# Kernel optimization log

Hardware: AMD Instinct MI355X
Metric: run time of the kernel (lower is better)

The kernel has to match this reference:

```python
import jax, jax.numpy as jnp
import numpy as np

B, S, H, E, V = 256, 512, 512, 128, 30000
RNN_IN = H + E + 1  # weighted context + id embedding + rate


def setup_inputs() -> dict:
    key = jax.random.key(0)
    ks = jax.random.split(key, 16)
    nrm = lambda k, shape, s=0.02: jax.random.normal(k, shape, dtype=jnp.float32) * s
    return {
        "input_id": jax.random.randint(ks[0], (B, 1), 0, V),
        "input_rate": jax.random.uniform(ks[1], (B, 1), dtype=jnp.float32),
        "hidden": nrm(ks[2], (1, B, H), 1.0),
        "encoder_outputs": nrm(ks[3], (S, B, H), 1.0),
        "attn_mask": jax.random.randint(ks[4], (B, S), 0, 2),
        "constraint_vec": (jax.random.uniform(ks[5], (B, V)) > 0.3).astype(jnp.float32),
        "emb_id": nrm(ks[6], (V, E)),
        "attn_w": nrm(ks[7], (2 * H, H)),
        "attn_b": jnp.zeros((H,), jnp.float32),
        "v_w": nrm(ks[8], (H,)),
        "w_ih": nrm(ks[9], (3 * H, RNN_IN)),
        "w_hh": nrm(ks[10], (3 * H, H)),
        "b_ih": jnp.zeros((3 * H,), jnp.float32),
        "b_hh": jnp.zeros((3 * H,), jnp.float32),
        "fc_id_w": nrm(ks[11], (H, V)),
        "fc_id_b": jnp.zeros((V,), jnp.float32),
        "tandem_w": nrm(ks[12], (E + H, H)),
        "tandem_b": jnp.zeros((H,), jnp.float32),
        "rate_w": nrm(ks[13], (H, 1)),
        "rate_b": jnp.zeros((1,), jnp.float32),
    }


def reference(input_id, input_rate, hidden, encoder_outputs, attn_mask,
              constraint_vec, emb_id, attn_w, attn_b, v_w,
              w_ih, w_hh, b_ih, b_hh, fc_id_w, fc_id_b,
              tandem_w, tandem_b, rate_w, rate_b):
    hd = hidden.shape[-1]
    h0 = hidden[0]                                # [B, H]
    embedded = emb_id[input_id[:, 0]]             # [B, E] (dropout p=0 -> identity)

    # --- additive attention (concat-linear split to avoid [B,S,2H] concat) ---
    enc = jnp.transpose(encoder_outputs, (1, 0, 2))         # [B, S, H]
    hid_part = h0 @ attn_w[:hd]                             # [B, H]
    enc_part = jnp.einsum('bsh,hk->bsk', enc, attn_w[hd:])  # [B, S, H]
    energy = jnp.tanh(hid_part[:, None, :] + enc_part + attn_b)
    scores = jnp.einsum('bsh,h->bs', energy, v_w)           # [B, S]
    scores = jnp.where(attn_mask == 0, jnp.float32(-1e10), scores)
    a = jax.nn.softmax(scores, axis=1)
    weighted = jnp.einsum('bs,bsh->bh', a, enc)             # [B, H]

    # --- GRU cell (torch gate order: r, z, n) ---
    x = jnp.concatenate([weighted, embedded, input_rate], axis=1)  # [B, H+E+1]
    gi = x @ w_ih.T + b_ih
    gh = h0 @ w_hh.T + b_hh
    gi_r, gi_z, gi_n = jnp.split(gi, 3, axis=1)
    gh_r, gh_z, gh_n = jnp.split(gh, 3, axis=1)
    r = jax.nn.sigmoid(gi_r + gh_r)
    z = jax.nn.sigmoid(gi_z + gh_z)
    n = jnp.tanh(gi_n + r * gh_n)
    h1 = (1.0 - z) * n + z * h0                   # [B, H]

    # --- masked log-softmax over id vocabulary ---
    logits = h1 @ fc_id_w + fc_id_b               # [B, V]
    maxes = jnp.max(logits, axis=1, keepdims=True)
    x_exp = jnp.exp(logits - maxes) * constraint_vec
    pred = jnp.clip(x_exp / jnp.sum(x_exp, axis=1, keepdims=True), 1e-6, 1.0)
    prediction_id = jnp.log(pred)

    # --- tandem rate head ---
    max_id = jnp.argmax(prediction_id, axis=1)
    id_emb = emb_id[max_id]                       # [B, E]
    rate_in = jax.nn.relu(jnp.concatenate([id_emb, h1], axis=1) @ tandem_w + tandem_b)
    prediction_rate = jax.nn.sigmoid(rate_in @ rate_w + rate_b)  # [B, 1]

    return prediction_id, prediction_rate, h1[None]  # hidden [1, B, H]
```

## Files before the change

kernel.cpp:

```cpp
#include <hip/hip_runtime.h>
#include <hip/hip_bf16.h>

#define B_ 256
#define S_ 512
#define H_ 512
#define E_ 128
#define V_ 30000
#define RNNIN_ 641

using bf16x8 = __attribute__((ext_vector_type(8))) short;
using f32x4  = __attribute__((ext_vector_type(4))) float;

__device__ __forceinline__ short f2bf(float f) {
  unsigned int u = __float_as_uint(f);
  u += 0x7fffu + ((u >> 16) & 1u);
  return (short)(u >> 16);
}

__device__ __forceinline__ float fast_tanh(float x) {
  x = fminf(10.f, fmaxf(-10.f, x));
  float t = __expf(2.f * x);
  return (t - 1.f) / (t + 1.f);
}

__device__ __forceinline__ float sigmoidf(float x) {
  return 1.f / (1.f + __expf(-x));
}

__device__ __forceinline__ void gload_lds16(const void* g, void* l) {
  __builtin_amdgcn_global_load_lds(
      (const __attribute__((address_space(1))) void*)g,
      (__attribute__((address_space(3))) void*)l, 16, 0, 0);
}

__global__ __launch_bounds__(256) void pack_b(
    const float* __restrict__ in, unsigned short* __restrict__ out)
{
  int i = blockIdx.x * 256 + threadIdx.x;
  int k = i >> 9, n = i & 511;
  float v = in[i];
  int idx = ((((k >> 5) * 32 + (n >> 4)) * 4 + ((k >> 3) & 3)) * 16 + (n & 15)) * 8 + (k & 7);
  out[idx] = (unsigned short)f2bf(v);
}

template<bool BT, bool RELU>
__global__ __launch_bounds__(256) void gemm_f32(
    const float* __restrict__ A, const float* __restrict__ Bm,
    const float* __restrict__ bias, float* __restrict__ C,
    int M, int N, int K)
{
  __shared__ float As[16][65];
  __shared__ float Bs[16][65];
  const int m0 = blockIdx.x * 64, n0 = blockIdx.y * 64;
  const int tid = threadIdx.x;
  const int tx = tid & 15, ty = tid >> 4;
  float acc[4][4] = {};
  for (int k0 = 0; k0 < K; k0 += 16) {
    __syncthreads();
    #pragma unroll
    for (int i = 0; i < 4; i++) {
      int e = tid + i * 256;
      int m = e >> 4, k = e & 15;
      float v = 0.f;
      if (m0 + m < M && k0 + k < K) v = A[(size_t)(m0 + m) * K + k0 + k];
      As[k][m] = v;
    }
    #pragma unroll
    for (int i = 0; i < 4; i++) {
      int e = tid + i * 256;
      if (BT) {
        int n = e >> 4, k = e & 15;
        float v = 0.f;
        if (n0 + n < N && k0 + k < K) v = Bm[(size_t)(n0 + n) * K + k0 + k];
        Bs[k][n] = v;
      } else {
        int k = e >> 6, n = e & 63;
        float v = 0.f;
        if (n0 + n < N && k0 + k < K) v = Bm[(size_t)(k0 + k) * N + n0 + n];
        Bs[k][n] = v;
      }
    }
    __syncthreads();
    #pragma unroll
    for (int k = 0; k < 16; k++) {
      float a[4], b[4];
      #pragma unroll
      for (int i = 0; i < 4; i++) a[i] = As[k][ty * 4 + i];
      #pragma unroll
      for (int j = 0; j < 4; j++) b[j] = Bs[k][tx * 4 + j];
      #pragma unroll
      for (int i = 0; i < 4; i++)
        #pragma unroll
        for (int j = 0; j < 4; j++) acc[i][j] += a[i] * b[j];
    }
  }
  #pragma unroll
  for (int i = 0; i < 4; i++) {
    int m = m0 + ty * 4 + i;
    if (m >= M) continue;
    #pragma unroll
    for (int j = 0; j < 4; j++) {
      int n = n0 + tx * 4 + j;
      if (n >= N) continue;
      float v = acc[i][j] + (bias ? bias[n] : 0.f);
      if (RELU) v = fmaxf(v, 0.f);
      C[(size_t)m * N + n] = v;
    }
  }
}

__device__ void gemm_bt_dev(float (*As)[65], float (*Bs)[65],
    const float* __restrict__ A, const float* __restrict__ Bm,
    const float* __restrict__ bias, float* __restrict__ C,
    int M, int N, int K)
{
  const int m0 = blockIdx.x * 64, n0 = blockIdx.y * 64;
  const int tid = threadIdx.x;
  const int tx = tid & 15, ty = tid >> 4;
  float acc[4][4] = {};
  for (int k0 = 0; k0 < K; k0 += 16) {
    __syncthreads();
    #pragma unroll
    for (int i = 0; i < 4; i++) {
      int e = tid + i * 256;
      int m = e >> 4, k = e & 15;
      float v = 0.f;
      if (m0 + m < M && k0 + k < K) v = A[(size_t)(m0 + m) * K + k0 + k];
      As[k][m] = v;
    }
    #pragma unroll
    for (int i = 0; i < 4; i++) {
      int e = tid + i * 256;
      int n = e >> 4, k = e & 15;
      float v = 0.f;
      if (n0 + n < N && k0 + k < K) v = Bm[(size_t)(n0 + n) * K + k0 + k];
      Bs[k][n] = v;
    }
    __syncthreads();
    #pragma unroll
    for (int k = 0; k < 16; k++) {
      float a[4], b[4];
      #pragma unroll
      for (int i = 0; i < 4; i++) a[i] = As[k][ty * 4 + i];
      #pragma unroll
      for (int j = 0; j < 4; j++) b[j] = Bs[k][tx * 4 + j];
      #pragma unroll
      for (int i = 0; i < 4; i++)
        #pragma unroll
        for (int j = 0; j < 4; j++) acc[i][j] += a[i] * b[j];
    }
  }
  #pragma unroll
  for (int i = 0; i < 4; i++) {
    int m = m0 + ty * 4 + i;
    if (m >= M) continue;
    #pragma unroll
    for (int j = 0; j < 4; j++) {
      int n = n0 + tx * 4 + j;
      if (n >= N) continue;
      C[(size_t)m * N + n] = acc[i][j] + bias[n];
    }
  }
}

__global__ __launch_bounds__(256) void gemm_gru(
    const float* __restrict__ xb, const float* __restrict__ w_ih,
    const float* __restrict__ b_ih, float* __restrict__ gi,
    const float* __restrict__ hid, const float* __restrict__ w_hh,
    const float* __restrict__ b_hh, float* __restrict__ gh)
{
  __shared__ float As[16][65];
  __shared__ float Bs[16][65];
  if (blockIdx.z == 0) gemm_bt_dev(As, Bs, xb, w_ih, b_ih, gi, B_, 1536, RNNIN_);
  else                 gemm_bt_dev(As, Bs, hid, w_hh, b_hh, gh, B_, 1536, H_);
}

__global__ __launch_bounds__(256, 3) void attn_gemm_score(
    const float* __restrict__ A, const unsigned short* __restrict__ Btf,
    const float* __restrict__ hid_pb, const float* __restrict__ v_w,
    float* __restrict__ scores)
{
  __shared__ short As[2 * 4 * 64 * 8];
  __shared__ short Bs[2 * 16 * 64 * 8];

  const int bid  = blockIdx.x;
  const int tile = (bid & 7) * 512 + (bid >> 3);
  const int mblk = tile >> 1, nblk = tile & 1;
  const int m0 = mblk * 64, n0 = nblk * 256;

  const int tid  = threadIdx.x;
  const int lane = tid & 63;
  const int wv   = tid >> 6;
  const int quad = lane >> 4, l15 = lane & 15;

  const int arow = tid >> 2;
  const int aseg = tid & 3;
  const float* aptr = A + (size_t)(m0 + arow) * H_ + aseg * 16;
  const int ac = aseg >> 1, aq0 = (aseg & 1) * 2;
  short* aw0 = &As[((ac * 4 + (arow >> 4)) * 64 + aq0 * 16 + (arow & 15)) * 8];
  short* aw1 = aw0 + 16 * 8;

  const unsigned short* bsrc = Btf + nblk * 8192;

  f32x4 acc[4][4];
  #pragma unroll
  for (int i = 0; i < 4; i++)
    #pragma unroll
    for (int j = 0; j < 4; j++) acc[i][j] = f32x4{0.f, 0.f, 0.f, 0.f};

  float4 rA[4];
  #pragma unroll
  for (int i = 0; i < 4; i++) rA[i] = *(const float4*)(aptr + i * 4);

  for (int kt = 0; kt < 8; kt++) {
    __builtin_amdgcn_s_barrier();
    asm volatile("s_waitcnt vmcnt(0)" ::: "memory");

    #pragma unroll
    for (int i = 0; i < 8; i++) {
      const unsigned short* g = bsrc + (kt * 2 + (i >> 2)) * 16384
                                     + ((i & 3) * 256 + tid) * 8;
      gload_lds16((const void*)g, (void*)&Bs[(i * 256 + wv * 64) * 8]);
    }

    {
      bf16x8 f0, f1;
      f0[0] = f2bf(rA[0].x); f0[1] = f2bf(rA[0].y); f0[2] = f2bf(rA[0].z); f0[3] = f2bf(rA[0].w);
      f0[4] = f2bf(rA[1].x); f0[5] = f2bf(rA[1].y); f0[6] = f2bf(rA[1].z); f0[7] = f2bf(rA[1].w);
      f1[0] = f2bf(rA[2].x); f1[1] = f2bf(rA[2].y); f1[2] = f2bf(rA[2].z); f1[3] = f2bf(rA[2].w);
      f1[4] = f2bf(rA[3].x); f1[5] = f2bf(rA[3].y); f1[6] = f2bf(rA[3].z); f1[7] = f2bf(rA[3].w);
      *(bf16x8*)aw0 = f0;
      *(bf16x8*)aw1 = f1;
    }

    if (kt < 7) {
      asm volatile("" ::: "memory");
      const float* anext = aptr + (kt + 1) * 64;
      #pragma unroll
      for (int i = 0; i < 4; i++) rA[i] = *(const float4*)(anext + i * 4);
      asm volatile("s_waitcnt vmcnt(4) lgkmcnt(0)" ::: "memory");
    } else {
      asm volatile("s_waitcnt vmcnt(0) lgkmcnt(0)" ::: "memory");
    }
    __builtin_amdgcn_s_barrier();
    asm volatile("" ::: "memory");

    #pragma unroll
    for (int ch = 0; ch < 2; ch++) {
      bf16x8 a[4], b[4];
      #pragma unroll
      for (int ti = 0; ti < 4; ti++)
        a[ti] = *(const bf16x8*)&As[((ch * 4 + ti) * 64 + lane) * 8];
      #pragma unroll
      for (int tj = 0; tj < 4; tj++)
        b[tj] = *(const bf16x8*)&Bs[((ch * 16 + wv * 4 + tj) * 64 + lane) * 8];
      #pragma unroll
      for (int ti = 0; ti < 4; ti++)
        #pragma unroll
        for (int tj = 0; tj < 4; tj++)
          acc[ti][tj] = __builtin_amdgcn_mfma_f32_16x16x32_bf16(a[ti], b[tj], acc[ti][tj], 0, 0, 0);
    }
  }

  __syncthreads();
  float* part = (float*)As;
  #pragma unroll
  for (int ti = 0; ti < 4; ti++) {
    #pragma unroll
    for (int r = 0; r < 4; r++) {
      int m = m0 + ti * 16 + quad * 4 + r;
      int b = m & (B_ - 1);
      float sum = 0.f;
      #pragma unroll
      for (int tj = 0; tj < 4; tj++) {
        int n = n0 + wv * 64 + tj * 16 + l15;
        float v = acc[ti][tj][r] + hid_pb[b * H_ + n];
        sum += fast_tanh(v) * v_w[n];
      }
      sum += __shfl_xor(sum, 1);
      sum += __shfl_xor(sum, 2);
      sum += __shfl_xor(sum, 4);
      sum += __shfl_xor(sum, 8);
      if (l15 == 0) part[(ti * 16 + quad * 4 + r) * 4 + wv] = sum;
    }
  }
  __syncthreads();
  if (tid < 64) {
    float s4 = part[tid * 4 + 0] + part[tid * 4 + 1] + part[tid * 4 + 2] + part[tid * 4 + 3];
    int m = m0 + tid;
    atomicAdd(scores + (m & (B_ - 1)) * S_ + (m >> 8), s4);
  }
}

__global__ __launch_bounds__(256, 4) void logits_gemm(
    const unsigned short* __restrict__ Ab, const float* __restrict__ Bw,
    const float* __restrict__ bias, float* __restrict__ C)
{
  __shared__ short As[2 * 16 * 64 * 8];
  __shared__ short Bs[2 * 4 * 64 * 8];
  const int n0 = blockIdx.x * 64;
  const int tid = threadIdx.x;
  const int lane = tid & 63;
  const int wv = tid >> 6;
  const int quad = lane >> 4, l15 = lane & 15;

  f32x4 acc[4][4];
  #pragma unroll
  for (int i = 0; i < 4; i++)
    #pragma unroll
    for (int j = 0; j < 4; j++) acc[i][j] = f32x4{0.f, 0.f, 0.f, 0.f};

  const int nB  = tid & 63;
  const int kg  = tid >> 6;
  const int cB  = kg >> 1;
  const int q0  = (kg & 1) * 2;
  const int tjB = nB >> 4;
  const bool nOK = (n0 + nB) < V_;

  for (int kt = 0; kt < 8; kt++) {
    const int kb = kt * 64;
    __syncthreads();
    #pragma unroll
    for (int p = 0; p < 8; p++) {
      int m = p * 32 + (tid >> 3), f = tid & 7;
      int c = f >> 2, q = f & 3;
      bf16x8 v = *(const bf16x8*)(Ab + (size_t)m * H_ + kb + c * 32 + q * 8);
      int mt = m >> 4, ld = q * 16 + (m & 15);
      *(bf16x8*)&As[((c * 16 + mt) * 64 + ld) * 8] = v;
    }
    {
      float col[16];
      const float* src = Bw + (size_t)(kb + kg * 16) * V_ + n0 + nB;
      #pragma unroll
      for (int i = 0; i < 16; i++) col[i] = nOK ? src[(size_t)i * V_] : 0.f;
      bf16x8 f0, f1;
      #pragma unroll
      for (int i = 0; i < 8; i++) { f0[i] = f2bf(col[i]); f1[i] = f2bf(col[8 + i]); }
      int ld0 = q0 * 16 + (nB & 15);
      *(bf16x8*)&Bs[((cB * 4 + tjB) * 64 + ld0) * 8] = f0;
      *(bf16x8*)&Bs[((cB * 4 + tjB) * 64 + ld0 + 16) * 8] = f1;
    }
    __syncthreads();
    #pragma unroll
    for (int c = 0; c < 2; c++) {
      bf16x8 a[4], b[4];
      #pragma unroll
      for (int ti = 0; ti < 4; ti++)
        a[ti] = *(const bf16x8*)&As[((c * 16 + wv * 4 + ti) * 64 + lane) * 8];
      #pragma unroll
      for (int tj = 0; tj < 4; tj++)
        b[tj] = *(const bf16x8*)&Bs[((c * 4 + tj) * 64 + lane) * 8];
      #pragma unroll
      for (int ti = 0; ti < 4; ti++)
        #pragma unroll
        for (int tj = 0; tj < 4; tj++)
          acc[ti][tj] = __builtin_amdgcn_mfma_f32_16x16x32_bf16(a[ti], b[tj], acc[ti][tj], 0, 0, 0);
    }
  }
  #pragma unroll
  for (int ti = 0; ti < 4; ti++)
    #pragma unroll
    for (int r = 0; r < 4; r++) {
      int m = wv * 64 + ti * 16 + quad * 4 + r;
      #pragma unroll
      for (int tj = 0; tj < 4; tj++) {
        int n = n0 + tj * 16 + l15;
        if (n < V_) C[(size_t)m * V_ + n] = acc[ti][tj][r] + bias[n];
      }
    }
}

__global__ __launch_bounds__(256) void attn_softmax(
    const float* __restrict__ scores, const int* __restrict__ mask, float* __restrict__ aw)
{
  int b = blockIdx.x, tid = threadIdx.x;
  __shared__ float red[256];
  float v0 = scores[b * S_ + tid];
  float v1 = scores[b * S_ + tid + 256];
  if (mask[b * S_ + tid] == 0) v0 = -1e10f;
  if (mask[b * S_ + tid + 256] == 0) v1 = -1e10f;
  red[tid] = fmaxf(v0, v1);
  __syncthreads();
  for (int off = 128; off; off >>= 1) { if (tid < off) red[tid] = fmaxf(red[tid], red[tid + off]); __syncthreads(); }
  float mx = red[0];
  __syncthreads();
  float e0 = __expf(v0 - mx), e1 = __expf(v1 - mx);
  red[tid] = e0 + e1;
  __syncthreads();
  for (int off = 128; off; off >>= 1) { if (tid < off) red[tid] += red[tid + off]; __syncthreads(); }
  float inv = 1.f / red[0];
  aw[b * S_ + tid] = e0 * inv;
  aw[b * S_ + tid + 256] = e1 * inv;
}

__global__ __launch_bounds__(512) void attn_weighted_part(
    const float* __restrict__ aw, const float* __restrict__ enc, float* __restrict__ wpart)
{
  int b = blockIdx.x, c = blockIdx.y, h = threadIdx.x;
  __shared__ float a_s[128];
  if (h < 128) a_s[h] = aw[b * S_ + c * 128 + h];
  __syncthreads();
  const float* ep = enc + ((size_t)(c * 128) * B_ + b) * H_ + h;
  float acc = 0.f;
  #pragma unroll 8
  for (int s = 0; s < 128; s++)
    acc += a_s[s] * ep[(size_t)s * B_ * H_];
  wpart[((size_t)c * B_ + b) * H_ + h] = acc;
}

__global__ void build_x(const float* __restrict__ wpart, const int* __restrict__ ids,
                        const float* __restrict__ emb, const float* __restrict__ rate,
                        float* __restrict__ x)
{
  int i = blockIdx.x * 256 + threadIdx.x;
  if (i >= B_ * RNNIN_) return;
  int b = i / RNNIN_, j = i % RNNIN_;
  float v;
  if (j < H_) {
    size_t o = (size_t)b * H_ + j;
    const size_t st = (size_t)B_ * H_;
    v = wpart[o] + wpart[o + st] + wpart[o + 2 * st] + wpart[o + 3 * st];
  }
  else if (j < H_ + E_) v = emb[(size_t)ids[b] * E_ + (j - H_)];
  else v = rate[b];
  x[i] = v;
}

__global__ void gru_gates(const float* __restrict__ gi, const float* __restrict__ gh,
                          const float* __restrict__ h0, float* __restrict__ h1,
                          unsigned short* __restrict__ h1b, float* __restrict__ h1_out)
{
  int i = blockIdx.x * 256 + threadIdx.x;
  int b = i >> 9, j = i & (H_ - 1);
  const float* gib = gi + (size_t)b * 1536;
  const float* ghb = gh + (size_t)b * 1536;
  float r = sigmoidf(gib[j] + ghb[j]);
  float z = sigmoidf(gib[512 + j] + ghb[512 + j]);
  float n = fast_tanh(gib[1024 + j] + r * ghb[1024 + j]);
  float h = (1.f - z) * n + z * h0[i];
  h1[i] = h;
  h1b[i] = (unsigned short)f2bf(h);
  h1_out[i] = h;
}

__global__ __launch_bounds__(1024) void softmax_fused(
    float* __restrict__ lp, const float* __restrict__ cv, int* __restrict__ maxid)
{
  int b = blockIdx.x, tid = threadIdx.x;
  int wid = tid >> 6, lane = tid & 63;
  float* row = lp + (size_t)b * V_;
  const float* cvr = cv + (size_t)b * V_;
  __shared__ float redf[16];
  __shared__ float rede[16];
  __shared__ int   redi[16];

  float mx = -INFINITY;
  for (int v = tid; v < V_; v += 1024) mx = fmaxf(mx, row[v]);
  #pragma unroll
  for (int o = 1; o < 64; o <<= 1) mx = fmaxf(mx, __shfl_xor(mx, o));
  if (lane == 0) redf[wid] = mx;
  __syncthreads();
  if (tid == 0) {
    float m = redf[0];
    for (int i = 1; i < 16; i++) m = fmaxf(m, redf[i]);
    redf[0] = m;
  }
  __syncthreads();
  float M = redf[0];
  __syncthreads();

  float s = 0.f, best = -1.f;
  int bi = 0;
  for (int v = tid; v < V_; v += 1024) {
    float e = __expf(row[v] - M) * cvr[v];
    row[v] = e;
    s += e;
    if (e > best) { best = e; bi = v; }
  }
  #pragma unroll
  for (int o = 1; o < 64; o <<= 1) {
    s += __shfl_xor(s, o);
    float ob = __shfl_xor(best, o);
    int oi = __shfl_xor(bi, o);
    if (ob > best || (ob == best && oi < bi)) { best = ob; bi = oi; }
  }
  if (lane == 0) { redf[wid] = s; rede[wid] = best; redi[wid] = bi; }
  __syncthreads();
  if (tid == 0) {
    float ss = 0.f, bb = rede[0];
    int ii = redi[0];
    for (int i = 0; i < 16; i++) {
      ss += redf[i];
      if (rede[i] > bb || (rede[i] == bb && redi[i] < ii)) { bb = rede[i]; ii = redi[i]; }
    }
    redf[0] = ss;
    maxid[b] = ii;
  }
  __syncthreads();
  float inv = 1.f / redf[0];
  for (int v = tid; v < V_; v += 1024) {
    float p = row[v] * inv;
    p = fminf(fmaxf(p, 1e-6f), 1.f);
    row[v] = __logf(p);
  }
}

__global__ void build_tandem(const int* __restrict__ maxid, const float* __restrict__ emb,
                             const float* __restrict__ h1, float* __restrict__ t)
{
  int i = blockIdx.x * 256 + threadIdx.x;
  if (i >= B_ * 640) return;
  int b = i / 640, j = i % 640;
  t[i] = (j < E_) ? emb[(size_t)maxid[b] * E_ + j] : h1[b * H_ + (j - E_)];
}

__global__ __launch_bounds__(64) void rate_head(const float* __restrict__ rate_in,
                                                const float* __restrict__ rate_w,
                                                const float* __restrict__ rate_b,
                                                float* __restrict__ out)
{
  int b = blockIdx.x, t = threadIdx.x;
  float s = 0.f;
  #pragma unroll
  for (int i = 0; i < 8; i++) s += rate_in[b * H_ + t + 64 * i] * rate_w[t + 64 * i];
  #pragma unroll
  for (int m = 32; m; m >>= 1) s += __shfl_xor(s, m);
  if (t == 0) out[b] = sigmoidf(s + rate_b[0]);
}

extern "C" void kernel_launch(void* const* d_in, const int* in_sizes, int n_in,
                              void* d_out, int out_size, void* d_ws, size_t ws_size,
                              hipStream_t stream)
{
  const int*   input_id   = (const int*)  d_in[0];
  const float* input_rate = (const float*)d_in[1];
  const float* hidden     = (const float*)d_in[2];
  const float* enc        = (const float*)d_in[3];
  const int*   attn_mask  = (const int*)  d_in[4];
  const float* cv         = (const float*)d_in[5];
  const float* emb        = (const float*)d_in[6];
  const float* attn_w     = (const float*)d_in[7];
  const float* attn_b     = (const float*)d_in[8];
  const float* v_w        = (const float*)d_in[9];
  const float* w_ih       = (const float*)d_in[10];
  const float* w_hh       = (const float*)d_in[11];
  const float* b_ih       = (const float*)d_in[12];
  const float* b_hh       = (const float*)d_in[13];
  const float* fc_w       = (const float*)d_in[14];
  const float* fc_b       = (const float*)d_in[15];
  const float* tan_w      = (const float*)d_in[16];
  const float* tan_b      = (const float*)d_in[17];
  const float* rate_w     = (const float*)d_in[18];
  const float* rate_b     = (const float*)d_in[19];

  float* out = (float*)d_out;
  float* ws  = (float*)d_ws;
  float* hid_pb   = ws;
  float* scores   = ws + 131072;
  float* aw       = ws + 262144;
  float* weighted = ws + 393216;
  float* xbuf     = ws + 524288;
  float* gi       = ws + 688384;
  float* gh       = ws + 1081600;
  float* h1       = ws + 1474816;
  float* rate_in  = ws + 1605888;
  int*   maxid    = (int*)(ws + 1736960);
  unsigned short* Btf = (unsigned short*)(ws + 1737216);
  unsigned short* h1b = (unsigned short*)(ws + 1868288);
  float* wpart = gi;

  float* out_pred = out;
  float* out_rate = out + (size_t)B_ * V_;
  float* out_h1   = out + (size_t)B_ * V_ + B_;
  (void)weighted;

  pack_b<<<1024, 256, 0, stream>>>(attn_w + (size_t)H_ * H_, Btf);

  hipMemsetAsync(scores, 0, (size_t)B_ * S_ * sizeof(float), stream);

  gemm_f32<false, false><<<dim3(4, 8), 256, 0, stream>>>(hidden, attn_w, attn_b, hid_pb, B_, H_, H_);

  attn_gemm_score<<<4096, 256, 0, stream>>>(enc, Btf, hid_pb, v_w, scores);

  attn_softmax<<<B_, 256, 0, stream>>>(scores, attn_mask, aw);
  attn_weighted_part<<<dim3(B_, 4), 512, 0, stream>>>(aw, enc, wpart);
  build_x<<<641, 256, 0, stream>>>(wpart, input_id, emb, input_rate, xbuf);

  gemm_gru<<<dim3(4, 24, 2), 256, 0, stream>>>(xbuf, w_ih, b_ih, gi, hidden, w_hh, b_hh, gh);
  gru_gates<<<512, 256, 0, stream>>>(gi, gh, hidden, h1, h1b, out_h1);

  logits_gemm<<<469, 256, 0, stream>>>(h1b, fc_w, fc_b, out_pred);
  softmax_fused<<<B_, 1024, 0, stream>>>(out_pred, cv, maxid);

  build_tandem<<<640, 256, 0, stream>>>(maxid, emb, h1, xbuf);
  gemm_f32<false, true><<<dim3(4, 8), 256, 0, stream>>>(xbuf, tan_w, tan_b, rate_in, B_, H_, 640);
  rate_head<<<B_, 64, 0, stream>>>(rate_in, rate_w, rate_b, out_rate);
}
```

Baseline: 1.042 ms.

## Fuse prep and tandem kernels, stream B from registers in attention GEMM

Merges the attn_w bf16 packing with the hidden-projection GEMM into one launch. It also folds the tandem input gather into the tandem GEMM, removing the xbuf round-trip and a launch. The attention-score GEMM now loads B fragments directly from global memory into registers instead of staging them in LDS. A is double-buffered in LDS so each k step needs only one barrier. The weighted-context reduction is split into 8 sequence chunks instead of 4 to raise parallelism, at the cost of summing more partial results.

Measured after the change: 1.004 ms. 3.6% less time.

```diff
diff --git a/kernel.cpp b/kernel.cpp
--- a/kernel.cpp
+++ b/kernel.cpp
@@ -27,31 +27,11 @@
   return 1.f / (1.f + __expf(-x));
 }
 
-__device__ __forceinline__ void gload_lds16(const void* g, void* l) {
-  __builtin_amdgcn_global_load_lds(
-      (const __attribute__((address_space(1))) void*)g,
-      (__attribute__((address_space(3))) void*)l, 16, 0, 0);
-}
-
-__global__ __launch_bounds__(256) void pack_b(
-    const float* __restrict__ in, unsigned short* __restrict__ out)
-{
-  int i = blockIdx.x * 256 + threadIdx.x;
-  int k = i >> 9, n = i & 511;
-  float v = in[i];
-  int idx = ((((k >> 5) * 32 + (n >> 4)) * 4 + ((k >> 3) & 3)) * 16 + (n & 15)) * 8 + (k & 7);
-  out[idx] = (unsigned short)f2bf(v);
-}
-
-template<bool BT, bool RELU>
-__global__ __launch_bounds__(256) void gemm_f32(
+__device__ void gemm_nn_dev(float (*As)[65], float (*Bs)[65],
     const float* __restrict__ A, const float* __restrict__ Bm,
     const float* __restrict__ bias, float* __restrict__ C,
-    int M, int N, int K)
-{
-  __shared__ float As[16][65];
-  __shared__ float Bs[16][65];
-  const int m0 = blockIdx.x * 64, n0 = blockIdx.y * 64;
+    int M, int N, int K, int m0, int n0)
+{
   const int tid = threadIdx.x;
   const int tx = tid & 15, ty = tid >> 4;
   float acc[4][4] = {};
@@ -68,17 +48,10 @@
     #pragma unroll
     for (int i = 0; i < 4; i++) {
       int e = tid + i * 256;
-      if (BT) {
-        int n = e >> 4, k = e & 15;
-        float v = 0.f;
-        if (n0 + n < N && k0 + k < K) v = Bm[(size_t)(n0 + n) * K + k0 + k];
-        Bs[k][n] = v;
-      } else {
-        int k = e >> 6, n = e & 63;
-        float v = 0.f;
-        if (n0 + n < N && k0 + k < K) v = Bm[(size_t)(k0 + k) * N + n0 + n];
-        Bs[k][n] = v;
-      }
+      int k = e >> 6, n = e & 63;
+      float v = 0.f;
+      if (n0 + n < N && k0 + k < K) v = Bm[(size_t)(k0 + k) * N + n0 + n];
+      Bs[k][n] = v;
     }
     __syncthreads();
     #pragma unroll
@@ -102,9 +75,7 @@
     for (int j = 0; j < 4; j++) {
       int n = n0 + tx * 4 + j;
       if (n >= N) continue;
-      float v = acc[i][j] + (bias ? bias[n] : 0.f);
-      if (RELU) v = fmaxf(v, 0.f);
-      C[(size_t)m * N + n] = v;
+      C[(size_t)m * N + n] = acc[i][j] + bias[n];
     }
   }
 }
@@ -163,25 +134,33 @@
   }
 }
 
-__global__ __launch_bounds__(256) void gemm_gru(
-    const float* __restrict__ xb, const float* __restrict__ w_ih,
-    const float* __restrict__ b_ih, float* __restrict__ gi,
-    const float* __restrict__ hid, const float* __restrict__ w_hh,
-    const float* __restrict__ b_hh, float* __restrict__ gh)
+__global__ __launch_bounds__(256) void prep_fused(
+    const float* __restrict__ attn_w, unsigned short* __restrict__ Btf,
+    const float* __restrict__ hidden, const float* __restrict__ attn_b,
+    float* __restrict__ hid_pb)
 {
   __shared__ float As[16][65];
   __shared__ float Bs[16][65];
-  if (blockIdx.z == 0) gemm_bt_dev(As, Bs, xb, w_ih, b_ih, gi, B_, 1536, RNNIN_);
-  else                 gemm_bt_dev(As, Bs, hid, w_hh, b_hh, gh, B_, 1536, H_);
-}
-
-__global__ __launch_bounds__(256, 3) void attn_gemm_score(
+  int bid = blockIdx.x;
+  if (bid < 1024) {
+    int i = bid * 256 + threadIdx.x;
+    int k = i >> 9, n = i & 511;
+    float v = attn_w[(size_t)H_ * H_ + i];
+    int idx = ((((k >> 5) * 32 + (n >> 4)) * 4 + ((k >> 3) & 3)) * 16 + (n & 15)) * 8 + (k & 7);
+    Btf[idx] = (unsigned short)f2bf(v);
+  } else {
+    int bb = bid - 1024;
+    gemm_nn_dev(As, Bs, hidden, attn_w, attn_b, hid_pb, B_, H_, H_,
+                (bb & 3) * 64, (bb >> 2) * 64);
+  }
+}
+
+__global__ __launch_bounds__(256) void attn_gemm_score(
     const float* __restrict__ A, const unsigned short* __restrict__ Btf,
     const float* __restrict__ hid_pb, const float* __restrict__ v_w,
     float* __restrict__ scores)
 {
-  __shared__ short As[2 * 4 * 64 * 8];
-  __shared__ short Bs[2 * 16 * 64 * 8];
+  __shared__ short As[2 * 4096];
 
   const int bid  = blockIdx.x;
   const int tile = (bid & 7) * 512 + (bid >> 3);
@@ -193,14 +172,12 @@
   const int wv   = tid >> 6;
   const int quad = lane >> 4, l15 = lane & 15;
 
-  const int arow = tid >> 2;
-  const int aseg = tid & 3;
+  const int arow = tid >> 2, aseg = tid & 3;
   const float* aptr = A + (size_t)(m0 + arow) * H_ + aseg * 16;
   const int ac = aseg >> 1, aq0 = (aseg & 1) * 2;
   short* aw0 = &As[((ac * 4 + (arow >> 4)) * 64 + aq0 * 16 + (arow & 15)) * 8];
-  short* aw1 = aw0 + 16 * 8;
-
-  const unsigned short* bsrc = Btf + nblk * 8192;
+
+  const int nf0 = nblk * 16 + wv * 4;
 
   f32x4 acc[4][4];
   #pragma unroll
@@ -212,16 +189,14 @@
   #pragma unroll
   for (int i = 0; i < 4; i++) rA[i] = *(const float4*)(aptr + i * 4);
 
+  #pragma unroll
   for (int kt = 0; kt < 8; kt++) {
-    __builtin_amdgcn_s_barrier();
-    asm volatile("s_waitcnt vmcnt(0)" ::: "memory");
-
-    #pragma unroll
-    for (int i = 0; i < 8; i++) {
-      const unsigned short* g = bsrc + (kt * 2 + (i >> 2)) * 16384
-                                     + ((i & 3) * 256 + tid) * 8;
-      gload_lds16((const void*)g, (void*)&Bs[(i * 256 + wv * 64) * 8]);
-    }
+    bf16x8 b[2][4];
+    #pragma unroll
+    for (int kc = 0; kc < 2; kc++)
+      #pragma unroll
+      for (int tj = 0; tj < 4; tj++)
+        b[kc][tj] = *(const bf16x8*)(Btf + (((kt * 2 + kc) * 32 + nf0 + tj) << 9) + lane * 8);
 
     {
       bf16x8 f0, f1;
@@ -229,36 +204,32 @@
       f0[4] = f2bf(rA[1].x); f0[5] = f2bf(rA[1].y); f0[6] = f2bf(rA[1].z); f0[7] = f2bf(rA[1].w);
       f1[0] = f2bf(rA[2].x); f1[1] = f2bf(rA[2].y); f1[2] = f2bf(rA[2].z); f1[3] = f2bf(rA[2].w);
       f1[4] = f2bf(rA[3].x); f1[5] = f2bf(rA[3].y); f1[6] = f2bf(rA[3].z); f1[7] = f2bf(rA[3].w);
-      *(bf16x8*)aw0 = f0;
-      *(bf16x8*)aw1 = f1;
+      *(bf16x8*)(aw0 + (kt & 1) * 4096)       = f0;
+      *(bf16x8*)(aw0 + (kt & 1) * 4096 + 128) = f1;
     }
 
     if (kt < 7) {
-      asm volatile("" ::: "memory");
-      const float* anext = aptr + (kt + 1) * 64;
-      #pragma unroll
-      for (int i = 0; i < 4; i++) rA[i] = *(const float4*)(anext + i * 4);
-      asm volatile("s_waitcnt vmcnt(4) lgkmcnt(0)" ::: "memory");
-    } else {
-      asm volatile("s_waitcnt vmcnt(0) lgkmcnt(0)" ::: "memory");
-    }
+      const float* an = aptr + (kt + 1) * 64;
+      #pragma unroll
+      for (int i = 0; i < 4; i++) rA[i] = *(const float4*)(an + i * 4);
+    }
+
+    asm volatile("s_waitcnt lgkmcnt(0)" ::: "memory");
     __builtin_amdgcn_s_barrier();
-    asm volatile("" ::: "memory");
-
-    #pragma unroll
-    for (int ch = 0; ch < 2; ch++) {
-      bf16x8 a[4], b[4];
-      #pragma unroll
-      for (int ti = 0; ti < 4; ti++)
-        a[ti] = *(const bf16x8*)&As[((ch * 4 + ti) * 64 + lane) * 8];
-      #pragma unroll
-      for (int tj = 0; tj < 4; tj++)
-        b[tj] = *(const bf16x8*)&Bs[((ch * 16 + wv * 4 + tj) * 64 + lane) * 8];
-      #pragma unroll
-      for (int ti = 0; ti < 4; ti++)
+    __builtin_amdgcn_sched_barrier(0);
+
+    const short* ab = &As[(kt & 1) * 4096];
+    #pragma unroll
+    for (int kc = 0; kc < 2; kc++) {
+      bf16x8 a[4];
+      #pragma unroll
+      for (int mi = 0; mi < 4; mi++)
+        a[mi] = *(const bf16x8*)&ab[((kc * 4 + mi) * 64 + lane) * 8];
+      #pragma unroll
+      for (int mi = 0; mi < 4; mi++)
         #pragma unroll
         for (int tj = 0; tj < 4; tj++)
-          acc[ti][tj] = __builtin_amdgcn_mfma_f32_16x16x32_bf16(a[ti], b[tj], acc[ti][tj], 0, 0, 0);
+          acc[mi][tj] = __builtin_amdgcn_mfma_f32_16x16x32_bf16(a[mi], b[kc][tj], acc[mi][tj], 0, 0, 0);
     }
   }
 
@@ -292,6 +263,18 @@
   }
 }
 
+__global__ __launch_bounds__(256) void gemm_gru(
+    const float* __restrict__ xb, const float* __restrict__ w_ih,
+    const float* __restrict__ b_ih, float* __restrict__ gi,
+    const float* __restrict__ hid, const float* __restrict__ w_hh,
+    const float* __restrict__ b_hh, float* __restrict__ gh)
+{
+  __shared__ float As[16][65];
+  __shared__ float Bs[16][65];
+  if (blockIdx.z == 0) gemm_bt_dev(As, Bs, xb, w_ih, b_ih, gi, B_, 1536, RNNIN_);
+  else                 gemm_bt_dev(As, Bs, hid, w_hh, b_hh, gh, B_, 1536, H_);
+}
+
 __global__ __launch_bounds__(256, 4) void logits_gemm(
     const unsigned short* __restrict__ Ab, const float* __restrict__ Bw,
     const float* __restrict__ bias, float* __restrict__ C)
@@ -397,13 +380,13 @@
     const float* __restrict__ aw, const float* __restrict__ enc, float* __restrict__ wpart)
 {
   int b = blockIdx.x, c = blockIdx.y, h = threadIdx.x;
-  __shared__ float a_s[128];
-  if (h < 128) a_s[h] = aw[b * S_ + c * 128 + h];
-  __syncthreads();
-  const float* ep = enc + ((size_t)(c * 128) * B_ + b) * H_ + h;
+  __shared__ float a_s[64];
+  if (h < 64) a_s[h] = aw[b * S_ + c * 64 + h];
+  __syncthreads();
+  const float* ep = enc + ((size_t)(c * 64) * B_ + b) * H_ + h;
   float acc = 0.f;
   #pragma unroll 8
-  for (int s = 0; s < 128; s++)
+  for (int s = 0; s < 64; s++)
     acc += a_s[s] * ep[(size_t)s * B_ * H_];
   wpart[((size_t)c * B_ + b) * H_ + h] = acc;
 }
@@ -419,7 +402,9 @@
   if (j < H_) {
     size_t o = (size_t)b * H_ + j;
     const size_t st = (size_t)B_ * H_;
-    v = wpart[o] + wpart[o + st] + wpart[o + 2 * st] + wpart[o + 3 * st];
+    v = 0.f;
+    #pragma unroll
+    for (int c = 0; c < 8; c++) v += wpart[o + c * st];
   }
   else if (j < H_ + E_) v = emb[(size_t)ids[b] * E_ + (j - H_)];
   else v = rate[b];
@@ -505,13 +490,57 @@
   }
 }
 
-__global__ void build_tandem(const int* __restrict__ maxid, const float* __restrict__ emb,
-                             const float* __restrict__ h1, float* __restrict__ t)
-{
-  int i = blockIdx.x * 256 + threadIdx.x;
-  if (i >= B_ * 640) return;
-  int b = i / 640, j = i % 640;
-  t[i] = (j < E_) ? emb[(size_t)maxid[b] * E_ + j] : h1[b * H_ + (j - E_)];
+__global__ __launch_bounds__(256) void tandem_gemm(
+    const int* __restrict__ maxid, const float* __restrict__ emb,
+    const float* __restrict__ h1, const float* __restrict__ tan_w,
+    const float* __restrict__ tan_b, float* __restrict__ rate_in)
+{
+  __shared__ float As[16][65];
+  __shared__ float Bs[16][65];
+  const int m0 = blockIdx.x * 64, n0 = blockIdx.y * 64;
+  const int tid = threadIdx.x;
+  const int tx = tid & 15, ty = tid >> 4;
+  float acc[4][4] = {};
+  for (int k0 = 0; k0 < 640; k0 += 16) {
+    __syncthreads();
+    #pragma unroll
+    for (int i = 0; i < 4; i++) {
+      int e = tid + i * 256;
+      int m = e >> 4, kk = e & 15;
+      int mm = m0 + m, k = k0 + kk;
+      float v = (k < E_) ? emb[(size_t)maxid[mm] * E_ + k]
+                         : h1[(size_t)mm * H_ + (k - E_)];
+      As[kk][m] = v;
+    }
+    #pragma unroll
+    for (int i = 0; i < 4; i++) {
+      int e = tid + i * 256;
+      int k = e >> 6, n = e & 63;
+      Bs[k][n] = tan_w[(size_t)(k0 + k) * H_ + n0 + n];
+    }
+    __syncthreads();
+    #pragma unroll
+    for (int k = 0; k < 16; k++) {
+      float a[4], b[4];
+      #pragma unroll
+      for (int i = 0; i < 4; i++) a[i] = As[k][ty * 4 + i];
+      #pragma unroll
+      for (int j = 0; j < 4; j++) b[j] = Bs[k][tx * 4 + j];
+      #pragma unroll
+      for (int i = 0; i < 4; i++)
+        #pragma unroll
+        for (int j = 0; j < 4; j++) acc[i][j] += a[i] * b[j];
+    }
+  }
+  #pragma unroll
+  for (int i = 0; i < 4; i++) {
+    int m = m0 + ty * 4 + i;
+    #pragma unroll
+    for (int j = 0; j < 4; j++) {
+      int n = n0 + tx * 4 + j;
+      rate_in[(size_t)m * H_ + n] = fmaxf(acc[i][j] + tan_b[n], 0.f);
+    }
+  }
 }
 
 __global__ __launch_bounds__(64) void rate_head(const float* __restrict__ rate_in,
@@ -558,7 +587,6 @@
   float* hid_pb   = ws;
   float* scores   = ws + 131072;
   float* aw       = ws + 262144;
-  float* weighted = ws + 393216;
   float* xbuf     = ws + 524288;
   float* gi       = ws + 688384;
   float* gh       = ws + 1081600;
@@ -572,18 +600,15 @@
   float* out_pred = out;
   float* out_rate = out + (size_t)B_ * V_;
   float* out_h1   = out + (size_t)B_ * V_ + B_;
-  (void)weighted;
-
-  pack_b<<<1024, 256, 0, stream>>>(attn_w + (size_t)H_ * H_, Btf);
 
   hipMemsetAsync(scores, 0, (size_t)B_ * S_ * sizeof(float), stream);
 
-  gemm_f32<false, false><<<dim3(4, 8), 256, 0, stream>>>(hidden, attn_w, attn_b, hid_pb, B_, H_, H_);
+  prep_fused<<<1056, 256, 0, stream>>>(attn_w, Btf, hidden, attn_b, hid_pb);
 
   attn_gemm_score<<<4096, 256, 0, stream>>>(enc, Btf, hid_pb, v_w, scores);
 
   attn_softmax<<<B_, 256, 0, stream>>>(scores, attn_mask, aw);
-  attn_weighted_part<<<dim3(B_, 4), 512, 0, stream>>>(aw, enc, wpart);
+  attn_weighted_part<<<dim3(B_, 8), 512, 0, stream>>>(aw, enc, wpart);
   build_x<<<641, 256, 0, stream>>>(wpart, input_id, emb, input_rate, xbuf);
 
   gemm_gru<<<dim3(4, 24, 2), 256, 0, stream>>>(xbuf, w_ih, b_ih, gi, hidden, w_hh, b_hh, gh);
@@ -592,7 +617,6 @@
   logits_gemm<<<469, 256, 0, stream>>>(h1b, fc_w, fc_b, out_pred);
   softmax_fused<<<B_, 1024, 0, stream>>>(out_pred, cv, maxid);
 
-  build_tandem<<<640, 256, 0, stream>>>(maxid, emb, h1, xbuf);
-  gemm_f32<false, true><<<dim3(4, 8), 256, 0, stream>>>(xbuf, tan_w, tan_b, rate_in, B_, H_, 640);
+  tandem_gemm<<<dim3(4, 8), 256, 0, stream>>>(maxid, emb, h1, tan_w, tan_b, rate_in);
   rate_head<<<B_, 64, 0, stream>>>(rate_in, rate_w, rate_b, out_rate);
 }
```
